# Kernel optimization log

Measured on AMD Instinct MI355X. Metric: run time of the kernel, lower is better.

Reference implementation:

```python
import jax, jax.numpy as jnp
import numpy as np

DIM = 768
HEADS = 12
HEAD_DIM = DIM // HEADS


def setup_inputs() -> dict:
    key = jax.random.key(0)
    ks = jax.random.split(key, 6)
    B, Nq, Nkv = 2, 2048, 2048
    s = 0.02
    return {
        "query_source": jax.random.normal(ks[0], (B, Nq, DIM), jnp.float32),
        "kv_source": jax.random.normal(ks[1], (B, Nkv, DIM), jnp.float32),
        "Wq": jax.random.normal(ks[2], (DIM, DIM), jnp.float32) * s,
        "Wkv": jax.random.normal(ks[3], (DIM, 2 * DIM), jnp.float32) * s,
        "Wproj": jax.random.normal(ks[4], (DIM, DIM), jnp.float32) * s,
        "bproj": jax.random.normal(ks[5], (DIM,), jnp.float32) * s,
    }


def reference(query_source, kv_source, Wq, Wkv, Wproj, bproj):
    B, Nq, D = query_source.shape
    Nkv = kv_source.shape[1]
    scale = HEAD_DIM ** -0.5
    # projections (qkv_bias=False)
    q = (query_source @ Wq).reshape(B, Nq, HEADS, HEAD_DIM)
    kv = (kv_source @ Wkv).reshape(B, Nkv, 2, HEADS, HEAD_DIM)
    k, v = kv[:, :, 0], kv[:, :, 1]  # (B, Nkv, H, Dh)
    # scores: (B, H, Nq, Nkv)
    attn = jnp.einsum("bqhd,bkhd->bhqk", q, k) * scale
    attn = jax.nn.softmax(attn, axis=-1)
    # attn_drop = 0 (eval)
    x = jnp.einsum("bhqk,bkhd->bqhd", attn, v).reshape(B, Nq, D)
    return x @ Wproj + bproj
```

## Files before the change

### kernel.cpp

```cpp
#include <hip/hip_runtime.h>
#include <math.h>
#include <stdint.h>

typedef __bf16 bf16_t;
typedef __attribute__((ext_vector_type(8))) __bf16 bf16x8;
typedef __attribute__((ext_vector_type(4))) __bf16 bf16x4;
typedef __attribute__((ext_vector_type(4))) float f32x4;

#define DIM   768
#define HEADS 12
#define HD    64
#define NB    2
#define NQ    2048
#define NKV   2048
#define MROWS 4096
#define NQKV  2304

__device__ __forceinline__ float fast_exp2(float x)
{
#if __has_builtin(__builtin_amdgcn_exp2f)
    return __builtin_amdgcn_exp2f(x);
#else
    return exp2f(x);
#endif
}

__device__ __forceinline__ uint32_t pack_bf16x2(float a, float b)
{
    const uint32_t lo = __builtin_bit_cast(uint32_t, a) + 0x8000u;
    const uint32_t hi = __builtin_bit_cast(uint32_t, b) + 0x8000u;
#if __has_builtin(__builtin_amdgcn_perm)
    return __builtin_amdgcn_perm(hi, lo, 0x07060302u);
#else
    return (lo >> 16) | (hi & 0xffff0000u);
#endif
}

__device__ __forceinline__ void async_copy16(const bf16_t* g, bf16_t* l)
{
    typedef const __attribute__((address_space(1))) uint32_t* gp_t;
    typedef __attribute__((address_space(3))) uint32_t* lp_t;
    __builtin_amdgcn_global_load_lds((gp_t)(const void*)g, (lp_t)(void*)l, 16, 0, 0);
}

__global__ void cast2_bf16(const float* __restrict__ a, bf16_t* __restrict__ oa,
                           const float* __restrict__ b, bf16_t* __restrict__ ob, int n)
{
    const float* in  = blockIdx.z ? b : a;
    bf16_t*      out = blockIdx.z ? ob : oa;
    int i = (blockIdx.x * blockDim.x + threadIdx.x) * 8;
    if (i >= n) return;
    bf16x8 v;
#pragma unroll
    for (int j = 0; j < 8; j++) v[j] = (bf16_t)in[i + j];
    *(bf16x8*)(out + i) = v;
}

__global__ void transpose_cast_all(const float* __restrict__ Wq, const float* __restrict__ Wkv,
                                   const float* __restrict__ Wproj, bf16_t* __restrict__ Wt)
{
    const int z = blockIdx.z;
    const float* W; bf16_t* T; int N;
    if (z == 0)      { W = Wq;    T = Wt;                        N = DIM; }
    else if (z == 1) { W = Wkv;   T = Wt + (size_t)DIM * DIM;    N = 2 * DIM; }
    else             { W = Wproj; T = Wt + (size_t)NQKV * DIM;   N = DIM; }
    const int n0 = blockIdx.x * 32;
    if (n0 >= N) return;
    const int k0 = blockIdx.y * 32;
    __shared__ float tile[32][33];
    const int tx = threadIdx.x & 31, ty = threadIdx.x >> 5;
#pragma unroll
    for (int i = 0; i < 4; i++)
        tile[ty + i * 8][tx] = W[(size_t)(k0 + ty + i * 8) * N + n0 + tx];
    __syncthreads();
#pragma unroll
    for (int i = 0; i < 4; i++)
        T[(size_t)(n0 + ty + i * 8) * DIM + k0 + tx] = (bf16_t)tile[tx][ty + i * 8];
}

template<int MODE, int TN>
__global__ __launch_bounds__(256)
void gemm_m97(const bf16_t* __restrict__ Aq, const bf16_t* __restrict__ Akv,
              const bf16_t* __restrict__ Bt,
              bf16_t* __restrict__ Qb, bf16_t* __restrict__ Kb, bf16_t* __restrict__ Vtb,
              float* __restrict__ ofp, const float* __restrict__ bias, float escale)
{
    constexpr int K  = DIM;
    constexpr int NT = TN / 32;
    constexpr int SELEMS = (MODE == 0) ? (128 * 136) : (128 * 32 + TN * 32);
    __shared__ bf16_t smem[SELEMS];
    bf16_t* As = smem;
    bf16_t* Bs = smem + 128 * 32;

    const int tid  = threadIdx.x;
    const int wave = tid >> 6, lane = tid & 63;
    const int quad = lane >> 4, l16 = lane & 15;
    const int bm = blockIdx.x * 128, bn = blockIdx.y * TN;
    const int wm = (wave >> 1) * 64, wn = (wave & 1) * (TN / 2);

    const bf16_t* A = (MODE == 0) ? (bn < DIM ? Aq : Akv) : Aq;

    const int srow = tid >> 2, scol = (tid & 3) * 8;
    const bf16_t* Ab = A  + (size_t)(bm + srow) * K + scol;
    const bf16_t* Bb = Bt + (size_t)(bn + srow) * K + scol;
    bf16_t* AsD0 = &As[srow * 32 + scol];
    bf16_t* AsD1 = &As[(srow + 64) * 32 + scol];
    bf16_t* BsD0 = &Bs[srow * 32 + scol];
    bf16_t* BsD1 = &Bs[(srow + 64) * 32 + scol];

    f32x4 acc[4][NT] = {};

    for (int k0 = 0; k0 < K; k0 += 32) {
        async_copy16(Ab + k0, AsD0);
        async_copy16(Ab + k0 + (size_t)64 * K, AsD1);
        async_copy16(Bb + k0, BsD0);
        if constexpr (TN == 128) async_copy16(Bb + k0 + (size_t)64 * K, BsD1);
        __syncthreads();
        bf16x8 af[4], bfr[NT];
#pragma unroll
        for (int mt = 0; mt < 4; mt++)
            af[mt] = *(const bf16x8*)(&As[(wm + mt * 16 + l16) * 32 + quad * 8]);
#pragma unroll
        for (int nt = 0; nt < NT; nt++)
            bfr[nt] = *(const bf16x8*)(&Bs[(wn + nt * 16 + l16) * 32 + quad * 8]);
#pragma unroll
        for (int mt = 0; mt < 4; mt++)
#pragma unroll
            for (int nt = 0; nt < NT; nt++)
                acc[mt][nt] = __builtin_amdgcn_mfma_f32_16x16x32_bf16(
                    af[mt], bfr[nt], acc[mt][nt], 0, 0, 0);
        __syncthreads();
    }

    if (MODE == 1) {
#pragma unroll
        for (int mt = 0; mt < 4; mt++)
#pragma unroll
            for (int nt = 0; nt < NT; nt++)
#pragma unroll
                for (int r = 0; r < 4; r++) {
                    const int gm = bm + wm + mt * 16 + quad * 4 + r;
                    const int gn = bn + wn + nt * 16 + l16;
                    ofp[(size_t)gm * DIM + gn] = acc[mt][nt][r] + bias[gn];
                }
    } else if (bn < DIM) {
#pragma unroll
        for (int mt = 0; mt < 4; mt++)
#pragma unroll
            for (int nt = 0; nt < NT; nt++)
#pragma unroll
                for (int r = 0; r < 4; r++) {
                    const int gm = bm + wm + mt * 16 + quad * 4 + r;
                    const int gn = bn + wn + nt * 16 + l16;
                    Qb[(size_t)gm * DIM + gn] = (bf16_t)(acc[mt][nt][r] * escale);
                }
    } else if (bn < 2 * DIM) {
#pragma unroll
        for (int mt = 0; mt < 4; mt++)
#pragma unroll
            for (int nt = 0; nt < NT; nt++)
#pragma unroll
                for (int r = 0; r < 4; r++) {
                    const int gm = bm + wm + mt * 16 + quad * 4 + r;
                    const int gn = bn + wn + nt * 16 + l16 - DIM;
                    Kb[(size_t)gm * DIM + gn] = (bf16_t)acc[mt][nt][r];
                }
    } else {
        bf16_t* tr = smem;
#pragma unroll
        for (int mt = 0; mt < 4; mt++)
#pragma unroll
            for (int nt = 0; nt < NT; nt++) {
                bf16x4 tv;
#pragma unroll
                for (int r = 0; r < 4; r++) tv[r] = (bf16_t)acc[mt][nt][r];
                *(bf16x4*)(&tr[(wn + nt * 16 + l16) * 136 + wm + mt * 16 + quad * 4]) = tv;
            }
        __syncthreads();
        const int b = bm >> 11, kv0 = bm & 2047;
        const int n2base = bn - 2 * DIM;
#pragma unroll
        for (int i = 0; i < 8; i++) {
            const int row = i * 16 + (tid >> 4);
            const int col = (tid & 15) * 8;
            const int n2 = n2base + row, h = n2 >> 6, d = n2 & 63;
            *(bf16x8*)(Vtb + ((size_t)(b * HEADS + h) * HD + d) * NKV + kv0 + col) =
                *(const bf16x8*)(&tr[row * 136 + col]);
        }
    }
}

__global__ __launch_bounds__(256, 3)
void attn_kernel(const bf16_t* __restrict__ Qb, const bf16_t* __restrict__ Kb,
                 const bf16_t* __restrict__ Vt, bf16_t* __restrict__ Xb)
{
    __shared__ __align__(16) bf16_t kvbuf[16384];
    __shared__ float libuf[4][2][16];

    const int tid  = threadIdx.x;
    const int wave = tid >> 6, lane = tid & 63;
    const int quad = lane >> 4, l16 = lane & 15;
    const int l7   = l16 & 7;
    const int qh = wave & 1, kvh = wave >> 1;
    const int bh = blockIdx.x;
    const int b = bh / HEADS, h = bh % HEADS;
    const int q0 = blockIdx.y * 64;

    const bf16_t* Qp = Qb + (size_t)b * NQ * DIM + h * HD;
    const bf16_t* Kp = Kb + (size_t)b * NKV * DIM + h * HD;
    const bf16_t* Vp = Vt + (size_t)(b * HEADS + h) * HD * NKV;

    bf16x8 qf[2][2];
#pragma unroll
    for (int qt = 0; qt < 2; qt++)
#pragma unroll
        for (int ks = 0; ks < 2; ks++)
            qf[qt][ks] = *(const bf16x8*)(Qp + (size_t)(q0 + qh * 32 + qt * 16 + l16) * DIM
                                          + ks * 32 + quad * 8);

    const int kl8 = lane >> 3;
    const bf16_t* Kg0 = Kp + (size_t)(wave * 32 + kl8) * DIM + (((lane & 7) ^ kl8) * 8);
    bf16_t* KgL = kvbuf + wave * 2048 + lane * 8;
    const int vl4 = lane >> 4, vp = lane & 15;
    const bf16_t* Vg0[4];
#pragma unroll
    for (int i = 0; i < 4; i++) {
        const int d  = wave * 16 + i * 4 + vl4;
        const int c  = (vp & 8) | ((vp & 7) ^ (d & 7));
        Vg0[i] = Vp + (size_t)d * NKV + c * 8;
    }
    bf16_t* VgL = kvbuf + 8192 + wave * 2048 + lane * 8;

    f32x4 o[4][2] = {};
    float li[2] = {0.0f, 0.0f};

    for (int t = 0; t < NKV / 128; t++) {
        const int kv0 = t * 128;
#pragma unroll
        for (int i = 0; i < 4; i++)
            async_copy16(Kg0 + (size_t)(kv0 + i * 8) * DIM, KgL + i * 512);
#pragma unroll
        for (int i = 0; i < 4; i++)
            async_copy16(Vg0[i] + kv0, VgL + i * 512);
        __syncthreads();

        f32x4 s[4][2] = {};
#pragma unroll
        for (int kt = 0; kt < 4; kt++)
#pragma unroll
            for (int ks = 0; ks < 2; ks++) {
                const bf16x8 kf = *(const bf16x8*)(&kvbuf[
                    (kvh * 64 + kt * 16 + l16) * 64 + ((((ks << 2) | quad) ^ l7) * 8)]);
#pragma unroll
                for (int qt = 0; qt < 2; qt++)
                    s[kt][qt] = __builtin_amdgcn_mfma_f32_16x16x32_bf16(
                        kf, qf[qt][ks], s[kt][qt], 0, 0, 0);
            }

        bf16x8 pb[2][2];
#pragma unroll
        for (int qt = 0; qt < 2; qt++) {
            float p[16];
#pragma unroll
            for (int kt = 0; kt < 4; kt++)
#pragma unroll
                for (int r = 0; r < 4; r++) p[kt * 4 + r] = fast_exp2(s[kt][qt][r]);
            float rs = 0.0f;
#pragma unroll
            for (int j = 0; j < 16; j++) rs += p[j];
            li[qt] += rs;
#pragma unroll
            for (int kc = 0; kc < 2; kc++) {
                union { uint32_t u[4]; bf16x8 v; } pu;
#pragma unroll
                for (int i = 0; i < 4; i++)
                    pu.u[i] = pack_bf16x2(p[kc * 8 + 2 * i], p[kc * 8 + 2 * i + 1]);
                pb[qt][kc] = pu.v;
            }
        }

#pragma unroll
        for (int dt = 0; dt < 4; dt++) {
            const int droff = 8192 + (dt * 16 + l16) * 128;
#pragma unroll
            for (int kc = 0; kc < 2; kc++) {
                const int c7 = kc * 4 + (quad >> 1);
                const int off = (quad & 1) * 4;
                const bf16x4 lo4 = *(const bf16x4*)(&kvbuf[
                    droff + (kvh * 8 + (c7 ^ l7)) * 8 + off]);
                const bf16x4 hi4 = *(const bf16x4*)(&kvbuf[
                    droff + (kvh * 8 + ((c7 + 2) ^ l7)) * 8 + off]);
                bf16x8 vf;
#pragma unroll
                for (int j = 0; j < 4; j++) { vf[j] = lo4[j]; vf[4 + j] = hi4[j]; }
#pragma unroll
                for (int qt = 0; qt < 2; qt++)
                    o[dt][qt] = __builtin_amdgcn_mfma_f32_16x16x32_bf16(
                        vf, pb[qt][kc], o[dt][qt], 0, 0, 0);
            }
        }
        __syncthreads();
    }

#pragma unroll
    for (int qt = 0; qt < 2; qt++) {
        li[qt] += __shfl_xor(li[qt], 16);
        li[qt] += __shfl_xor(li[qt], 32);
    }
    if (quad == 0) { libuf[wave][0][l16] = li[0]; libuf[wave][1][l16] = li[1]; }

    float* ob = (float*)(kvbuf + qh * 8192);
    if (kvh == 1) {
#pragma unroll
        for (int dt = 0; dt < 4; dt++)
#pragma unroll
            for (int qt = 0; qt < 2; qt++)
#pragma unroll
                for (int r = 0; r < 4; r++)
                    ob[(dt * 16 + quad * 4 + r) * 33 + qt * 16 + l16] = o[dt][qt][r];
    }
    __syncthreads();
    if (kvh == 0) {
        const float inv0 = 1.0f / (li[0] + libuf[2 + qh][0][l16]);
        const float inv1 = 1.0f / (li[1] + libuf[2 + qh][1][l16]);
#pragma unroll
        for (int dt = 0; dt < 4; dt++)
#pragma unroll
            for (int qt = 0; qt < 2; qt++)
#pragma unroll
                for (int r = 0; r < 4; r++)
                    o[dt][qt][r] = (o[dt][qt][r]
                                    + ob[(dt * 16 + quad * 4 + r) * 33 + qt * 16 + l16])
                                   * (qt ? inv1 : inv0);
    }
    __syncthreads();
    bf16_t* Ob16 = kvbuf;
    if (kvh == 0) {
#pragma unroll
        for (int dt = 0; dt < 4; dt++)
#pragma unroll
            for (int qt = 0; qt < 2; qt++) {
                bf16x4 ov;
#pragma unroll
                for (int r = 0; r < 4; r++) ov[r] = (bf16_t)o[dt][qt][r];
                *(bf16x4*)(&Ob16[(qh * 32 + qt * 16 + l16) * 72 + dt * 16 + quad * 4]) = ov;
            }
    }
    __syncthreads();
    {
        const int row = tid >> 2, ch = (tid & 3) * 16;
        bf16_t* dst = Xb + (size_t)(b * NQ + q0 + row) * DIM + h * HD + ch;
        *(bf16x8*)(dst)     = *(const bf16x8*)(&Ob16[row * 72 + ch]);
        *(bf16x8*)(dst + 8) = *(const bf16x8*)(&Ob16[row * 72 + ch + 8]);
    }
}

extern "C" void kernel_launch(void* const* d_in, const int* in_sizes, int n_in,
                              void* d_out, int out_size, void* d_ws, size_t ws_size,
                              hipStream_t stream)
{
    const float* qs    = (const float*)d_in[0];
    const float* kvs   = (const float*)d_in[1];
    const float* Wq    = (const float*)d_in[2];
    const float* Wkv   = (const float*)d_in[3];
    const float* Wproj = (const float*)d_in[4];
    const float* bproj = (const float*)d_in[5];
    float* out = (float*)d_out;

    bf16_t* w = (bf16_t*)d_ws;
    bf16_t* qs_bf  = w;  w += (size_t)MROWS * DIM;
    bf16_t* kvs_bf = w;  w += (size_t)MROWS * DIM;
    bf16_t* Wt     = w;  w += (size_t)NQKV * DIM;
    bf16_t* Wprojt = w;  w += (size_t)DIM * DIM;
    bf16_t* Qb     = w;  w += (size_t)MROWS * DIM;
    bf16_t* Kb     = w;  w += (size_t)MROWS * DIM;
    bf16_t* Vtb    = w;  w += (size_t)MROWS * DIM;
    bf16_t* Xb     = qs_bf;

    const int n1 = MROWS * DIM;
    cast2_bf16<<<dim3(n1 / 8 / 256, 1, 2), 256, 0, stream>>>(qs, qs_bf, kvs, kvs_bf, n1);
    transpose_cast_all<<<dim3(48, 24, 3), 256, 0, stream>>>(Wq, Wkv, Wproj, Wt);

    const float escale = 0.125f * 1.44269504088896341f;
    gemm_m97<0, 128><<<dim3(MROWS / 128, NQKV / 128), 256, 0, stream>>>(
        qs_bf, kvs_bf, Wt, Qb, Kb, Vtb, nullptr, nullptr, escale);
    attn_kernel<<<dim3(NB * HEADS, NQ / 64), 256, 0, stream>>>(Qb, Kb, Vtb, Xb);
    gemm_m97<1, 64><<<dim3(MROWS / 128, DIM / 64), 256, 0, stream>>>(
        Xb, nullptr, Wprojt, nullptr, nullptr, nullptr, out, bproj, 1.0f);
}
```

Before: 163.8 us.

## Double GEMM K-tile to 64 with XOR-swizzled LDS and permute V layout

The projection GEMMs now stage 64-wide K slices per iteration with an XOR swizzle on the LDS column, halving the number of barrier pairs and loop iterations while avoiding bank conflicts. The V-transpose epilogue writes kv columns in a permuted order so that the attention kernel can read its V fragment with a single 16-byte LDS load instead of two 8-byte loads and a register shuffle. The larger tile raises shared memory use per block, which could reduce occupancy.

```diff
diff --git a/kernel.cpp b/kernel.cpp
--- a/kernel.cpp
+++ b/kernel.cpp
@@ -80,55 +80,66 @@
 
 template<int MODE, int TN>
 __global__ __launch_bounds__(256)
-void gemm_m97(const bf16_t* __restrict__ Aq, const bf16_t* __restrict__ Akv,
-              const bf16_t* __restrict__ Bt,
-              bf16_t* __restrict__ Qb, bf16_t* __restrict__ Kb, bf16_t* __restrict__ Vtb,
-              float* __restrict__ ofp, const float* __restrict__ bias, float escale)
+void gemm_bk64(const bf16_t* __restrict__ Aq, const bf16_t* __restrict__ Akv,
+               const bf16_t* __restrict__ Bt,
+               bf16_t* __restrict__ Qb, bf16_t* __restrict__ Kb, bf16_t* __restrict__ Vtb,
+               float* __restrict__ ofp, const float* __restrict__ bias, float escale)
 {
     constexpr int K  = DIM;
     constexpr int NT = TN / 32;
-    constexpr int SELEMS = (MODE == 0) ? (128 * 136) : (128 * 32 + TN * 32);
-    __shared__ bf16_t smem[SELEMS];
+    constexpr int ABLK = 128 * 64;
+    constexpr int BBLK = TN * 64;
+    constexpr int SELEMS = (MODE == 0) ? (128 * 136) : (ABLK + BBLK);
+    __shared__ __align__(16) bf16_t smem[SELEMS];
     bf16_t* As = smem;
-    bf16_t* Bs = smem + 128 * 32;
+    bf16_t* Bs = smem + ABLK;
 
     const int tid  = threadIdx.x;
     const int wave = tid >> 6, lane = tid & 63;
-    const int quad = lane >> 4, l16 = lane & 15;
+    const int quad = lane >> 4, l16 = lane & 15, l7 = l16 & 7;
     const int bm = blockIdx.x * 128, bn = blockIdx.y * TN;
     const int wm = (wave >> 1) * 64, wn = (wave & 1) * (TN / 2);
 
     const bf16_t* A = (MODE == 0) ? (bn < DIM ? Aq : Akv) : Aq;
 
-    const int srow = tid >> 2, scol = (tid & 3) * 8;
-    const bf16_t* Ab = A  + (size_t)(bm + srow) * K + scol;
-    const bf16_t* Bb = Bt + (size_t)(bn + srow) * K + scol;
-    bf16_t* AsD0 = &As[srow * 32 + scol];
-    bf16_t* AsD1 = &As[(srow + 64) * 32 + scol];
-    bf16_t* BsD0 = &Bs[srow * 32 + scol];
-    bf16_t* BsD1 = &Bs[(srow + 64) * 32 + scol];
+    const int srow = tid >> 3;
+    const int scol = ((tid & 7) ^ (srow & 7)) * 8;
+    const bf16_t* Ag[4];
+    const bf16_t* Bg[NT];
+#pragma unroll
+    for (int i = 0; i < 4; i++)
+        Ag[i] = A + (size_t)(bm + i * 32 + srow) * K + scol;
+#pragma unroll
+    for (int i = 0; i < NT; i++)
+        Bg[i] = Bt + (size_t)(bn + i * 32 + srow) * K + scol;
+    bf16_t* AsL = As + tid * 8;
+    bf16_t* BsL = Bs + tid * 8;
 
     f32x4 acc[4][NT] = {};
 
-    for (int k0 = 0; k0 < K; k0 += 32) {
-        async_copy16(Ab + k0, AsD0);
-        async_copy16(Ab + k0 + (size_t)64 * K, AsD1);
-        async_copy16(Bb + k0, BsD0);
-        if constexpr (TN == 128) async_copy16(Bb + k0 + (size_t)64 * K, BsD1);
-        __syncthreads();
-        bf16x8 af[4], bfr[NT];
-#pragma unroll
-        for (int mt = 0; mt < 4; mt++)
-            af[mt] = *(const bf16x8*)(&As[(wm + mt * 16 + l16) * 32 + quad * 8]);
-#pragma unroll
-        for (int nt = 0; nt < NT; nt++)
-            bfr[nt] = *(const bf16x8*)(&Bs[(wn + nt * 16 + l16) * 32 + quad * 8]);
-#pragma unroll
-        for (int mt = 0; mt < 4; mt++)
+    for (int k0 = 0; k0 < K; k0 += 64) {
+#pragma unroll
+        for (int i = 0; i < 4; i++) async_copy16(Ag[i] + k0, AsL + i * 2048);
+#pragma unroll
+        for (int i = 0; i < NT; i++) async_copy16(Bg[i] + k0, BsL + i * 2048);
+        __syncthreads();
+#pragma unroll
+        for (int ks = 0; ks < 2; ks++) {
+            const int pc = ((ks * 4 + quad) ^ l7) * 8;
+            bf16x8 af[4], bfr[NT];
+#pragma unroll
+            for (int mt = 0; mt < 4; mt++)
+                af[mt] = *(const bf16x8*)(&As[(wm + mt * 16 + l16) * 64 + pc]);
 #pragma unroll
             for (int nt = 0; nt < NT; nt++)
-                acc[mt][nt] = __builtin_amdgcn_mfma_f32_16x16x32_bf16(
-                    af[mt], bfr[nt], acc[mt][nt], 0, 0, 0);
+                bfr[nt] = *(const bf16x8*)(&Bs[(wn + nt * 16 + l16) * 64 + pc]);
+#pragma unroll
+            for (int mt = 0; mt < 4; mt++)
+#pragma unroll
+                for (int nt = 0; nt < NT; nt++)
+                    acc[mt][nt] = __builtin_amdgcn_mfma_f32_16x16x32_bf16(
+                        af[mt], bfr[nt], acc[mt][nt], 0, 0, 0);
+        }
         __syncthreads();
     }
 
@@ -179,13 +190,17 @@
         __syncthreads();
         const int b = bm >> 11, kv0 = bm & 2047;
         const int n2base = bn - 2 * DIM;
+        const int cg = tid & 15, cc = cg >> 2, cq = cg & 3;
 #pragma unroll
         for (int i = 0; i < 8; i++) {
             const int row = i * 16 + (tid >> 4);
-            const int col = (tid & 15) * 8;
             const int n2 = n2base + row, h = n2 >> 6, d = n2 & 63;
-            *(bf16x8*)(Vtb + ((size_t)(b * HEADS + h) * HD + d) * NKV + kv0 + col) =
-                *(const bf16x8*)(&tr[row * 136 + col]);
+            const bf16x4 lo4 = *(const bf16x4*)(&tr[row * 136 + cc * 32 + cq * 4]);
+            const bf16x4 hi4 = *(const bf16x4*)(&tr[row * 136 + cc * 32 + 16 + cq * 4]);
+            bf16x8 vv;
+#pragma unroll
+            for (int j = 0; j < 4; j++) { vv[j] = lo4[j]; vv[4 + j] = hi4[j]; }
+            *(bf16x8*)(Vtb + ((size_t)(b * HEADS + h) * HD + d) * NKV + kv0 + cg * 8) = vv;
         }
     }
 }
@@ -225,8 +240,8 @@
     const bf16_t* Vg0[4];
 #pragma unroll
     for (int i = 0; i < 4; i++) {
-        const int d  = wave * 16 + i * 4 + vl4;
-        const int c  = (vp & 8) | ((vp & 7) ^ (d & 7));
+        const int d = wave * 16 + i * 4 + vl4;
+        const int c = (vp & 8) | ((vp & 7) ^ (d & 7));
         Vg0[i] = Vp + (size_t)d * NKV + c * 8;
     }
     bf16_t* VgL = kvbuf + 8192 + wave * 2048 + lane * 8;
@@ -284,15 +299,8 @@
             const int droff = 8192 + (dt * 16 + l16) * 128;
 #pragma unroll
             for (int kc = 0; kc < 2; kc++) {
-                const int c7 = kc * 4 + (quad >> 1);
-                const int off = (quad & 1) * 4;
-                const bf16x4 lo4 = *(const bf16x4*)(&kvbuf[
-                    droff + (kvh * 8 + (c7 ^ l7)) * 8 + off]);
-                const bf16x4 hi4 = *(const bf16x4*)(&kvbuf[
-                    droff + (kvh * 8 + ((c7 + 2) ^ l7)) * 8 + off]);
-                bf16x8 vf;
-#pragma unroll
-                for (int j = 0; j < 4; j++) { vf[j] = lo4[j]; vf[4 + j] = hi4[j]; }
+                const bf16x8 vf = *(const bf16x8*)(&kvbuf[
+                    droff + (kvh * 8 + ((kc * 4 + quad) ^ l7)) * 8]);
 #pragma unroll
                 for (int qt = 0; qt < 2; qt++)
                     o[dt][qt] = __builtin_amdgcn_mfma_f32_16x16x32_bf16(
@@ -382,9 +390,9 @@
     transpose_cast_all<<<dim3(48, 24, 3), 256, 0, stream>>>(Wq, Wkv, Wproj, Wt);
 
     const float escale = 0.125f * 1.44269504088896341f;
-    gemm_m97<0, 128><<<dim3(MROWS / 128, NQKV / 128), 256, 0, stream>>>(
+    gemm_bk64<0, 128><<<dim3(MROWS / 128, NQKV / 128), 256, 0, stream>>>(
         qs_bf, kvs_bf, Wt, Qb, Kb, Vtb, nullptr, nullptr, escale);
     attn_kernel<<<dim3(NB * HEADS, NQ / 64), 256, 0, stream>>>(Qb, Kb, Vtb, Xb);
-    gemm_m97<1, 64><<<dim3(MROWS / 128, DIM / 64), 256, 0, stream>>>(
+    gemm_bk64<1, 64><<<dim3(MROWS / 128, DIM / 64), 256, 0, stream>>>(
         Xb, nullptr, Wprojt, nullptr, nullptr, nullptr, out, bproj, 1.0f);
 }
```

New measurement: 161.0 us. About the same (-1.7%).
